# Performance work log

Hardware: AMD Instinct MI355X
Metric: run time of the kernel (lower is better)

## Reference

```python
import jax, jax.numpy as jnp
import numpy as np

B, L, D_IN = 2048, 512, 32
PRED_LEN = 96
COND = 128      # cond_dim (z_dim)
XPROJ = 128     # x_proj_dim defaults to cond_dim
ODE_H = 128     # ode_hidden
TDIM = 128      # time_dim
HID = 256       # hidden of final MLP
N_STEPS = 32    # fixed-step RK4 steps over t in [0,1] (stands in for adaptive dopri5)
LN_EPS = 1e-5


def _linear(x, w, b):
    return x @ w.T + b


def _layernorm(x, g, b):
    mu = jnp.mean(x, axis=-1, keepdims=True)
    var = jnp.var(x, axis=-1, keepdims=True)
    return (x - mu) * jax.lax.rsqrt(var + LN_EPS) * g + b


def _interp(x_seq, t):
    # linear interp over sequence dim: x_seq (B,L,D), scalar t in [0,1] -> (B,D)
    Ls = x_seq.shape[1]
    pos = jnp.clip(t, 0.0, 1.0) * (Ls - 1)
    i0 = jnp.clip(jnp.floor(pos).astype(jnp.int32), 0, Ls - 1)
    i1 = jnp.clip(i0 + 1, 0, Ls - 1)
    w = (pos - i0.astype(pos.dtype))
    x0 = jax.lax.dynamic_index_in_dim(x_seq, i0, axis=1, keepdims=False)
    x1 = jax.lax.dynamic_index_in_dim(x_seq, i1, axis=1, keepdims=False)
    return (1.0 - w) * x0 + w * x1


def setup_inputs() -> dict:
    key = jax.random.key(0)
    ks = jax.random.split(key, 16)

    def kaiming(k, shape):
        return jax.random.normal(k, shape, jnp.float32) * np.float32(np.sqrt(2.0 / shape[-1]))

    IN_F = PRED_LEN * D_IN + COND + TDIM   # 3328
    OUT_F = PRED_LEN * D_IN                # 3072
    return {
        "x_t": jax.random.normal(ks[0], (B, PRED_LEN, D_IN), jnp.float32),
        "past": jax.random.normal(ks[1], (B, L, D_IN), jnp.float32),
        "t": jax.random.randint(ks[2], (B,), 0, 1000),
        "xproj_w": kaiming(ks[3], (XPROJ, D_IN)), "xproj_b": jnp.zeros((XPROJ,), jnp.float32),
        "z0_w": kaiming(ks[4], (COND, XPROJ)), "z0_b": jnp.zeros((COND,), jnp.float32),
        "ln_g": jnp.ones((COND,), jnp.float32), "ln_b": jnp.zeros((COND,), jnp.float32),
        "w1": kaiming(ks[5], (ODE_H, COND + XPROJ)), "b1": jnp.zeros((ODE_H,), jnp.float32),
        "w2": kaiming(ks[6], (ODE_H, ODE_H)), "b2": jnp.zeros((ODE_H,), jnp.float32),
        "w3": kaiming(ks[7], (COND, ODE_H)), "b3": jnp.zeros((COND,), jnp.float32),
        "fw1": kaiming(ks[8], (HID, IN_F)), "fb1": jnp.zeros((HID,), jnp.float32),
        "fw2": kaiming(ks[9], (HID, HID)), "fb2": jnp.zeros((HID,), jnp.float32),
        "fw3": kaiming(ks[10], (OUT_F, HID)), "fb3": jnp.zeros((OUT_F,), jnp.float32),
    }


def _time_emb(t):
    half = TDIM // 2
    freqs = jnp.exp(-np.float32(np.log(10000.0)) * jnp.arange(half, dtype=jnp.float32) / (half - 1))
    args = t.astype(jnp.float32)[:, None] * freqs[None, :]
    return jnp.concatenate([jnp.sin(args), jnp.cos(args)], axis=1)  # (B, TDIM)


def _forward(x_t, past, t, xproj_w, xproj_b, z0_w, z0_b, ln_g, ln_b,
             w1, b1, w2, b2, w3, b3, fw1, fb1, fw2, fb2, fw3, fb3):
    Bn = x_t.shape[0]
    x_seq = _linear(past, xproj_w, xproj_b)           # (B,L,XPROJ)
    z0 = _linear(x_seq[:, 0, :], z0_w, z0_b)          # (B,COND)

    def odef(tt, z):
        xt = _interp(x_seq, tt)                       # (B,XPROJ)
        zn = _layernorm(z, ln_g, ln_b)
        h = jnp.concatenate([zn, xt], axis=-1)
        h = jax.nn.silu(_linear(h, w1, b1))
        h = jax.nn.silu(_linear(h, w2, b2))
        return _linear(h, w3, b3)                     # (B,COND)

    dt = jnp.float32(1.0 / N_STEPS)

    def step(z, tt):
        k1 = odef(tt, z)
        k2 = odef(tt + dt * 0.5, z + dt * 0.5 * k1)
        k3 = odef(tt + dt * 0.5, z + dt * 0.5 * k2)
        k4 = odef(tt + dt, z + dt * k3)
        return z + (dt / 6.0) * (k1 + 2.0 * k2 + 2.0 * k3 + k4), None

    ts = jnp.arange(N_STEPS, dtype=jnp.float32) * dt
    cond, _ = jax.lax.scan(step, z0, ts)              # zT (B,COND)

    temb = _time_emb(t)                               # (B,TDIM)
    x_flat = x_t.reshape(Bn, -1)                      # (B,PRED_LEN*D_IN)
    h = jnp.concatenate([x_flat, cond, temb], axis=1)
    h = jax.nn.silu(_linear(h, fw1, fb1))
    h = jax.nn.silu(_linear(h, fw2, fb2))
    eps = _linear(h, fw3, fb3)
    return eps.reshape(Bn, PRED_LEN, D_IN)


def reference(x_t, past, t, xproj_w, xproj_b, z0_w, z0_b, ln_g, ln_b,
              w1, b1, w2, b2, w3, b3, fw1, fb1, fw2, fb2, fw3, fb3):
    return _forward(x_t, past, t, xproj_w, xproj_b, z0_w, z0_b, ln_g, ln_b,
                    w1, b1, w2, b2, w3, b3, fw1, fb1, fw2, fb2, fw3, fb3)
```

## Files before the change

### kernel.cpp

```cpp
#include <hip/hip_runtime.h>
#include <math.h>

typedef _Float16 h8f16 __attribute__((ext_vector_type(8)));
typedef _Float16 h2f16 __attribute__((ext_vector_type(2)));
typedef float f32x4 __attribute__((ext_vector_type(4)));

#define MFMA16(a, b, c) __builtin_amdgcn_mfma_f32_16x16x32_f16((a), (b), (c), 0, 0, 0)

__device__ __forceinline__ float silu_f(float v) {
    return v * __builtin_amdgcn_rcpf(1.0f + __expf(-v));
}

__device__ __forceinline__ void bar_lds() {
    asm volatile("s_waitcnt lgkmcnt(0)" ::: "memory");
    __builtin_amdgcn_s_barrier();
    __builtin_amdgcn_sched_barrier(0);
}

__global__ __launch_bounds__(512, 1) void fat_kernel(
    const float* __restrict__ past,
    const float* __restrict__ xproj_w, const float* __restrict__ xproj_b,
    const float* __restrict__ z0_w, const float* __restrict__ z0_b,
    const float* __restrict__ ln_g, const float* __restrict__ ln_b,
    const float* __restrict__ w1, const float* __restrict__ b1,
    const float* __restrict__ w2, const float* __restrict__ b2,
    const float* __restrict__ w3, const float* __restrict__ b3,
    const float* __restrict__ x_t, const int* __restrict__ tvals,
    const float* __restrict__ fw1, const float* __restrict__ fw2,
    const float* __restrict__ fw3,
    float* __restrict__ zbuf, _Float16* __restrict__ hcat,
    _Float16* __restrict__ fw1h, _Float16* __restrict__ fw2h,
    _Float16* __restrict__ fw3h)
{
    __shared__ _Float16 hbuf[16][136];
    __shared__ _Float16 h1S[16][136];
    __shared__ _Float16 h2S[16][136];
    __shared__ float    pS[16][33];
    __shared__ float    x0S[16][128];
    __shared__ float    zS0[16][129];

    const int tid = threadIdx.x;

    if (blockIdx.x >= 128) {
        const int fid = blockIdx.x - 128;
        for (long c = fid * 512 + tid; c < 1032192; c += 104 * 512) {
            if (c < 786432) {
                const long b = c / 384, q = (c % 384) * 8;
                const float* s = x_t + b * 3072 + q;
                const f32x4 u0 = *(const f32x4*)s;
                const f32x4 u1 = *(const f32x4*)(s + 4);
                h8f16 v;
#pragma unroll
                for (int j = 0; j < 4; ++j) { v[j] = (_Float16)u0[j]; v[4 + j] = (_Float16)u1[j]; }
                *(h8f16*)&hcat[b * 3328 + q] = v;
            } else if (c < 819200) {
                const long u = c - 786432;
                const long b = u >> 4;
                const int j0 = (int)(u & 15) * 8;
                const float tv = (float)tvals[b];
                h8f16 v;
#pragma unroll
                for (int j = 0; j < 8; ++j) {
                    const int jj  = j0 + j;
                    const int idx = (jj < 64) ? jj : jj - 64;
                    const float fr = expf(-9.210340371976184f * (float)idx * (1.0f / 63.0f));
                    const float a  = tv * fr;
                    v[j] = (_Float16)((jj < 64) ? sinf(a) : cosf(a));
                }
                *(h8f16*)&hcat[b * 3328 + 3200 + j0] = v;
            } else {
                const float* src; _Float16* dst; long off;
                if (c < 925696)      { src = fw1; dst = fw1h; off = (c - 819200) * 8; }
                else if (c < 933888) { src = fw2; dst = fw2h; off = (c - 925696) * 8; }
                else                 { src = fw3; dst = fw3h; off = (c - 933888) * 8; }
                const f32x4 u0 = *(const f32x4*)(src + off);
                const f32x4 u1 = *(const f32x4*)(src + off + 4);
                h8f16 v;
#pragma unroll
                for (int j = 0; j < 4; ++j) { v[j] = (_Float16)u0[j]; v[4 + j] = (_Float16)u1[j]; }
                *(h8f16*)&dst[off] = v;
            }
        }
        return;
    }

    const int wid  = tid >> 6;
    const int lane = tid & 63;
    const int lrow = lane & 15;
    const int lhi  = lane >> 4;
    const int b0   = blockIdx.x * 16;
    const int nc   = wid * 16 + lrow;
    const int koff = lhi * 8;

    h8f16 w1f[4], wcf, w2f[4], w3f[4];
    float b1t, b2r, b3r;
    {
#pragma unroll
        for (int ks = 0; ks < 4; ++ks) {
            h8f16 v1, v2, v3;
#pragma unroll
            for (int j = 0; j < 8; ++j) {
                const int k = ks * 32 + koff + j;
                v1[j] = (_Float16)(w1[nc * 256 + k] * ln_g[k]);
                v2[j] = (_Float16)w2[nc * 128 + k];
                v3[j] = (_Float16)w3[nc * 128 + k];
            }
            w1f[ks] = v1; w2f[ks] = v2; w3f[ks] = v3;
        }
        float wc[8] = {0, 0, 0, 0, 0, 0, 0, 0};
        float bc = 0.0f, bb = 0.0f;
        const float* w1a = w1 + nc * 256;
        const float* w1b = w1a + 128;
#pragma unroll 4
        for (int k = 0; k < 128; ++k) {
            const float a = w1b[k];
            bc += a * xproj_b[k];
            bb += w1a[k] * ln_b[k];
            const float* xr = xproj_w + k * 32 + koff;
#pragma unroll
            for (int j = 0; j < 8; ++j) wc[j] += a * xr[j];
        }
        h8f16 v;
#pragma unroll
        for (int j = 0; j < 8; ++j) v[j] = (_Float16)wc[j];
        wcf = v;
        b1t = b1[nc] + bc + bb;
        b2r = b2[nc]; b3r = b3[nc];
    }

    pS[tid >> 5][tid & 31] = past[(long)(b0 + (tid >> 5)) * 16384 + (tid & 31)];
    __syncthreads();
    {
        const int r  = tid >> 5;
        const int c0 = (tid & 31) * 4;
#pragma unroll
        for (int cc = 0; cc < 4; ++cc) {
            const int kc = c0 + cc;
            float s = xproj_b[kc];
            const float* xr = xproj_w + kc * 32;
#pragma unroll
            for (int c = 0; c < 32; ++c) s += pS[r][c] * xr[c];
            x0S[r][kc] = s;
        }
    }
    __syncthreads();
    {
        const int nn = tid & 127;
        const int r0 = (tid >> 7) * 4;
        for (int p = 0; p < 4; ++p) {
            const int r = r0 + p;
            float s = z0_b[nn];
            const float* zr = z0_w + nn * 128;
            for (int k = 0; k < 128; ++k) s += x0S[r][k] * zr[k];
            zS0[r][nn] = s;
        }
    }
    __syncthreads();

    float zc[4], krk[4];
#pragma unroll
    for (int j = 0; j < 4; ++j) {
        zc[j] = zS0[4 * lhi + j][nc];
        hbuf[4 * lhi + j][nc] = (_Float16)zc[j];
    }

    const float DT = 1.0f / 32.0f;

    f32x4 s0a, s0b, s1a, s1b;
    auto stage = [&](int e) {
        const float pos = (float)e * 7.984375f;
        const int i0 = (int)pos;
        const int i1 = (i0 < 511) ? i0 + 1 : 511;
        const float* base = past + (long)(b0 + lrow) * 16384;
        const float* p0 = base + i0 * 32 + koff;
        const float* p1 = base + i1 * 32 + koff;
        s0a = *(const f32x4*)p0; s0b = *(const f32x4*)(p0 + 4);
        s1a = *(const f32x4*)p1; s1b = *(const f32x4*)(p1 + 4);
    };
    auto blend = [&](int e) -> h8f16 {
        const float pos = (float)e * 7.984375f;
        const float w = pos - floorf(pos);
        h8f16 r;
#pragma unroll
        for (int j = 0; j < 4; ++j) {
            r[j]     = (_Float16)(s0a[j] + w * (s1a[j] - s0a[j]));
            r[4 + j] = (_Float16)(s0b[j] + w * (s1b[j] - s0b[j]));
        }
        return r;
    };

    const h2f16 one2 = {(_Float16)1.0f, (_Float16)1.0f};

    auto phaseA = [&](h8f16 bxc) {
        h8f16 xf[4];
#pragma unroll
        for (int ks = 0; ks < 4; ++ks)
            xf[ks] = *(const h8f16*)&hbuf[lrow][ks * 32 + koff];
        float s0 = 0.f, s1 = 0.f, q0 = 0.f, q1 = 0.f;
#pragma unroll
        for (int ks = 0; ks < 4; ++ks) {
#pragma unroll
            for (int p = 0; p < 4; ++p) {
                const h2f16 x2 = {xf[ks][2 * p], xf[ks][2 * p + 1]};
                if (p & 1) {
                    s1 = __builtin_amdgcn_fdot2(x2, one2, s1, false);
                    q1 = __builtin_amdgcn_fdot2(x2, x2, q1, false);
                } else {
                    s0 = __builtin_amdgcn_fdot2(x2, one2, s0, false);
                    q0 = __builtin_amdgcn_fdot2(x2, x2, q0, false);
                }
            }
        }
        float s = s0 + s1, q = q0 + q1;
        s += __shfl_xor(s, 16); q += __shfl_xor(q, 16);
        s += __shfl_xor(s, 32); q += __shfl_xor(q, 32);
        const float mu  = s * (1.0f / 128.0f);
        const float var = q * (1.0f / 128.0f) - mu * mu;
        const float inv = 1.0f / sqrtf(var + 1e-5f);
        const _Float16 ih = (_Float16)inv;
        const _Float16 mh = (_Float16)(-mu * inv);
        h8f16 ip, mp;
#pragma unroll
        for (int j = 0; j < 8; ++j) { ip[j] = ih; mp[j] = mh; }
        f32x4 acc = {0, 0, 0, 0};
#pragma unroll
        for (int ks = 0; ks < 4; ++ks) {
            const h8f16 az = xf[ks] * ip + mp;
            acc = MFMA16(az, w1f[ks], acc);
        }
        acc = MFMA16(bxc, wcf, acc);
#pragma unroll
        for (int j = 0; j < 4; ++j)
            h1S[4 * lhi + j][nc] = (_Float16)silu_f(acc[j] + b1t);
    };
    auto phaseB = [&]() {
        f32x4 acc = {0, 0, 0, 0};
#pragma unroll
        for (int ks = 0; ks < 4; ++ks) {
            const h8f16 a = *(const h8f16*)&h1S[lrow][ks * 32 + koff];
            acc = MFMA16(a, w2f[ks], acc);
        }
#pragma unroll
        for (int j = 0; j < 4; ++j)
            h2S[4 * lhi + j][nc] = (_Float16)silu_f(acc[j] + b2r);
    };
    auto phaseC = [&]() -> f32x4 {
        f32x4 acc = {0, 0, 0, 0};
#pragma unroll
        for (int ks = 0; ks < 4; ++ks) {
            const h8f16 a = *(const h8f16*)&h2S[lrow][ks * 32 + koff];
            acc = MFMA16(a, w3f[ks], acc);
        }
#pragma unroll
        for (int j = 0; j < 4; ++j) acc[j] += b3r;
        return acc;
    };

    stage(0);
    h8f16 bxc = blend(0);
    __syncthreads();

#pragma unroll 1
    for (int st = 0; st < 32; ++st) {
        const int e1 = 2 * st + 1, e2 = 2 * st + 2;
        phaseA(bxc);
        stage(e1);
        bar_lds();
        phaseB(); bar_lds();
        {
            const f32x4 k = phaseC();
#pragma unroll
            for (int j = 0; j < 4; ++j) {
                krk[j] = k[j];
                hbuf[4 * lhi + j][nc] = (_Float16)(zc[j] + 0.5f * DT * k[j]);
            }
        }
        bar_lds();
        bxc = blend(e1);
        phaseA(bxc); bar_lds();
        phaseB(); bar_lds();
        {
            const f32x4 k = phaseC();
#pragma unroll
            for (int j = 0; j < 4; ++j) {
                krk[j] += 2.0f * k[j];
                hbuf[4 * lhi + j][nc] = (_Float16)(zc[j] + 0.5f * DT * k[j]);
            }
        }
        bar_lds();
        phaseA(bxc);
        stage(e2);
        bar_lds();
        phaseB(); bar_lds();
        {
            const f32x4 k = phaseC();
#pragma unroll
            for (int j = 0; j < 4; ++j) {
                krk[j] += 2.0f * k[j];
                hbuf[4 * lhi + j][nc] = (_Float16)(zc[j] + DT * k[j]);
            }
        }
        bar_lds();
        bxc = blend(e2);
        phaseA(bxc); bar_lds();
        phaseB(); bar_lds();
        {
            const f32x4 k = phaseC();
#pragma unroll
            for (int j = 0; j < 4; ++j) {
                zc[j] += (DT / 6.0f) * (krk[j] + k[j]);
                hbuf[4 * lhi + j][nc] = (_Float16)zc[j];
            }
        }
        bar_lds();
    }

#pragma unroll
    for (int j = 0; j < 4; ++j)
        zbuf[(long)(b0 + 4 * lhi + j) * 128 + nc] = zc[j];
}

__global__ __launch_bounds__(256) void gemm1z_kernel(
    const _Float16* __restrict__ hcat, const float* __restrict__ cond,
    const _Float16* __restrict__ fw1h, const float* __restrict__ fb1,
    _Float16* __restrict__ h1)
{
    __shared__ _Float16 aS[64][40];
    __shared__ _Float16 wS[64][40];
    const int mb = blockIdx.x * 64, nb = blockIdx.y * 64;
    const int tid = threadIdx.x, lane = tid & 63, wq = tid >> 6;
    const int lrow = lane & 15, lhi = lane >> 4;
    f32x4 acc[4];
#pragma unroll
    for (int nt = 0; nt < 4; ++nt) acc[nt] = (f32x4){0, 0, 0, 0};

    const int sr = tid >> 2;
    const int sk = (tid & 3) * 8;

    for (int k0 = 0; k0 < 3328; k0 += 32) {
        if (k0 >= 3072 && k0 < 3200) {
            const float* s = cond + (long)(mb + sr) * 128 + (k0 - 3072) + sk;
            const f32x4 u0 = *(const f32x4*)s;
            const f32x4 u1 = *(const f32x4*)(s + 4);
            h8f16 v;
#pragma unroll
            for (int j = 0; j < 4; ++j) { v[j] = (_Float16)u0[j]; v[4 + j] = (_Float16)u1[j]; }
            *(h8f16*)&aS[sr][sk] = v;
        } else {
            *(h8f16*)&aS[sr][sk] =
                *(const h8f16*)&hcat[(long)(mb + sr) * 3328 + k0 + sk];
        }
        *(h8f16*)&wS[sr][sk] = *(const h8f16*)&fw1h[(long)(nb + sr) * 3328 + k0 + sk];
        __syncthreads();
        const h8f16 a = *(const h8f16*)&aS[wq * 16 + lrow][lhi * 8];
#pragma unroll
        for (int nt = 0; nt < 4; ++nt) {
            const h8f16 bfr = *(const h8f16*)&wS[nt * 16 + lrow][lhi * 8];
            acc[nt] = MFMA16(a, bfr, acc[nt]);
        }
        __syncthreads();
    }

#pragma unroll
    for (int nt = 0; nt < 4; ++nt) {
        const int cc = nb + nt * 16 + lrow;
        const float bv = fb1[cc];
#pragma unroll
        for (int j = 0; j < 4; ++j) {
            const int rr = mb + wq * 16 + lhi * 4 + j;
            h1[(long)rr * 256 + cc] = (_Float16)silu_f(acc[nt][j] + bv);
        }
    }
}

template <bool SILU, bool OUT_F16>
__global__ __launch_bounds__(256) void gemm_ff(
    const _Float16* __restrict__ A, const _Float16* __restrict__ W,
    const float* __restrict__ bias, void* __restrict__ out,
    int M, int N, int K)
{
    __shared__ _Float16 aS[64][40];
    __shared__ _Float16 wS[64][40];
    const int mb = blockIdx.x * 64, nb = blockIdx.y * 64;
    const int tid = threadIdx.x, lane = tid & 63, wq = tid >> 6;
    const int lrow = lane & 15, lhi = lane >> 4;
    f32x4 acc[4];
#pragma unroll
    for (int nt = 0; nt < 4; ++nt) acc[nt] = (f32x4){0, 0, 0, 0};

    const int sr = tid >> 2;
    const int sk = (tid & 3) * 8;

    for (int k0 = 0; k0 < K; k0 += 32) {
        *(h8f16*)&aS[sr][sk] = *(const h8f16*)&A[(long)(mb + sr) * K + k0 + sk];
        *(h8f16*)&wS[sr][sk] = *(const h8f16*)&W[(long)(nb + sr) * K + k0 + sk];
        __syncthreads();
        const h8f16 a = *(const h8f16*)&aS[wq * 16 + lrow][lhi * 8];
#pragma unroll
        for (int nt = 0; nt < 4; ++nt) {
            const h8f16 bfr = *(const h8f16*)&wS[nt * 16 + lrow][lhi * 8];
            acc[nt] = MFMA16(a, bfr, acc[nt]);
        }
        __syncthreads();
    }

#pragma unroll
    for (int nt = 0; nt < 4; ++nt) {
        const int cc = nb + nt * 16 + lrow;
        const float bv = bias[cc];
#pragma unroll
        for (int j = 0; j < 4; ++j) {
            const int rr = mb + wq * 16 + lhi * 4 + j;
            float v = acc[nt][j] + bv;
            if (SILU) v = silu_f(v);
            if (OUT_F16) ((_Float16*)out)[(long)rr * N + cc] = (_Float16)v;
            else         ((float*)out)[(long)rr * N + cc] = v;
        }
    }
}

extern "C" void kernel_launch(void* const* d_in, const int* in_sizes, int n_in,
                              void* d_out, int out_size, void* d_ws, size_t ws_size,
                              hipStream_t stream)
{
    const float* x_t     = (const float*)d_in[0];
    const float* past    = (const float*)d_in[1];
    const int*   tvals   = (const int*)d_in[2];
    const float* xproj_w = (const float*)d_in[3];
    const float* xproj_b = (const float*)d_in[4];
    const float* z0_w    = (const float*)d_in[5];
    const float* z0_b    = (const float*)d_in[6];
    const float* ln_g    = (const float*)d_in[7];
    const float* ln_b    = (const float*)d_in[8];
    const float* w1      = (const float*)d_in[9];
    const float* b1      = (const float*)d_in[10];
    const float* w2      = (const float*)d_in[11];
    const float* b2      = (const float*)d_in[12];
    const float* w3      = (const float*)d_in[13];
    const float* b3      = (const float*)d_in[14];
    const float* fw1     = (const float*)d_in[15];
    const float* fb1     = (const float*)d_in[16];
    const float* fw2     = (const float*)d_in[17];
    const float* fb2     = (const float*)d_in[18];
    const float* fw3     = (const float*)d_in[19];
    const float* fb3     = (const float*)d_in[20];

    char* ws = (char*)d_ws;
    float*     zbuf = (float*)ws;
    _Float16*  hcat = (_Float16*)(ws + (1 << 20));
    _Float16*  h1   = (_Float16*)(ws + 15 * (1 << 20));
    _Float16*  h2   = (_Float16*)(ws + 16 * (1 << 20));
    _Float16*  fw1h = (_Float16*)(ws + 17 * (1 << 20));
    _Float16*  fw2h = (_Float16*)(ws + 19 * (1 << 20));
    _Float16*  fw3h = (_Float16*)(ws + 20 * (1 << 20));

    fat_kernel<<<232, 512, 0, stream>>>(past, xproj_w, xproj_b, z0_w, z0_b,
                                        ln_g, ln_b, w1, b1, w2, b2, w3, b3,
                                        x_t, tvals, fw1, fw2, fw3,
                                        zbuf, hcat, fw1h, fw2h, fw3h);

    gemm1z_kernel<<<dim3(32, 4), 256, 0, stream>>>(hcat, zbuf, fw1h, fb1, h1);

    gemm_ff<true,  true ><<<dim3(32, 4),  256, 0, stream>>>(h1, fw2h, fb2, h2, 2048, 256, 256);
    gemm_ff<false, false><<<dim3(32, 48), 256, 0, stream>>>(h2, fw3h, fb3, d_out, 2048, 3072, 256);
}
```

Baseline: 297.8 us.

## Fuse second and third feed-forward GEMMs with h2 kept in LDS

Merges the two final MLP GEMMs into one kernel. Each block computes the SiLU hidden tile for its 64 rows into shared memory, then streams fw3 tiles against it to write six 64-column output tiles. This drops one kernel launch and the global write and read of h2. In exchange, the 256x256 layer is recomputed once per column-group block, and the output GEMM runs on far fewer blocks with longer serial loops, so there is less parallelism for hiding latency.

After: 315.4 us. 5.9% more time.

```diff
diff --git a/kernel.cpp b/kernel.cpp
--- a/kernel.cpp
+++ b/kernel.cpp
@@ -373,48 +373,73 @@
     }
 }
 
-template <bool SILU, bool OUT_F16>
-__global__ __launch_bounds__(256) void gemm_ff(
-    const _Float16* __restrict__ A, const _Float16* __restrict__ W,
-    const float* __restrict__ bias, void* __restrict__ out,
-    int M, int N, int K)
+__global__ __launch_bounds__(256) void gemm23_kernel(
+    const _Float16* __restrict__ h1, const _Float16* __restrict__ fw2h,
+    const float* __restrict__ fb2, const _Float16* __restrict__ fw3h,
+    const float* __restrict__ fb3, float* __restrict__ out)
 {
     __shared__ _Float16 aS[64][40];
     __shared__ _Float16 wS[64][40];
-    const int mb = blockIdx.x * 64, nb = blockIdx.y * 64;
+    __shared__ _Float16 h2T[64][264];
+    const int mb = blockIdx.x * 64;
+    const int n3base = blockIdx.y * 384;
     const int tid = threadIdx.x, lane = tid & 63, wq = tid >> 6;
     const int lrow = lane & 15, lhi = lane >> 4;
-    f32x4 acc[4];
-#pragma unroll
-    for (int nt = 0; nt < 4; ++nt) acc[nt] = (f32x4){0, 0, 0, 0};
-
     const int sr = tid >> 2;
     const int sk = (tid & 3) * 8;
 
-    for (int k0 = 0; k0 < K; k0 += 32) {
-        *(h8f16*)&aS[sr][sk] = *(const h8f16*)&A[(long)(mb + sr) * K + k0 + sk];
-        *(h8f16*)&wS[sr][sk] = *(const h8f16*)&W[(long)(nb + sr) * K + k0 + sk];
+    for (int nb2 = 0; nb2 < 256; nb2 += 64) {
+        f32x4 acc[4];
+#pragma unroll
+        for (int nt = 0; nt < 4; ++nt) acc[nt] = (f32x4){0, 0, 0, 0};
+        for (int k0 = 0; k0 < 256; k0 += 32) {
+            *(h8f16*)&aS[sr][sk] = *(const h8f16*)&h1[(long)(mb + sr) * 256 + k0 + sk];
+            *(h8f16*)&wS[sr][sk] = *(const h8f16*)&fw2h[(long)(nb2 + sr) * 256 + k0 + sk];
+            __syncthreads();
+            const h8f16 a = *(const h8f16*)&aS[wq * 16 + lrow][lhi * 8];
+#pragma unroll
+            for (int nt = 0; nt < 4; ++nt) {
+                const h8f16 bfr = *(const h8f16*)&wS[nt * 16 + lrow][lhi * 8];
+                acc[nt] = MFMA16(a, bfr, acc[nt]);
+            }
+            __syncthreads();
+        }
+#pragma unroll
+        for (int nt = 0; nt < 4; ++nt) {
+            const int cc = nb2 + nt * 16 + lrow;
+            const float bv = fb2[cc];
+#pragma unroll
+            for (int j = 0; j < 4; ++j)
+                h2T[wq * 16 + lhi * 4 + j][cc] = (_Float16)silu_f(acc[nt][j] + bv);
+        }
         __syncthreads();
-        const h8f16 a = *(const h8f16*)&aS[wq * 16 + lrow][lhi * 8];
+    }
+
+    for (int nt3 = 0; nt3 < 384; nt3 += 64) {
+        const int nb3 = n3base + nt3;
+        f32x4 acc[4];
+#pragma unroll
+        for (int nt = 0; nt < 4; ++nt) acc[nt] = (f32x4){0, 0, 0, 0};
+        for (int k0 = 0; k0 < 256; k0 += 32) {
+            *(h8f16*)&wS[sr][sk] = *(const h8f16*)&fw3h[(long)(nb3 + sr) * 256 + k0 + sk];
+            __syncthreads();
+            const h8f16 a = *(const h8f16*)&h2T[wq * 16 + lrow][k0 + lhi * 8];
+#pragma unroll
+            for (int nt = 0; nt < 4; ++nt) {
+                const h8f16 bfr = *(const h8f16*)&wS[nt * 16 + lrow][lhi * 8];
+                acc[nt] = MFMA16(a, bfr, acc[nt]);
+            }
+            __syncthreads();
+        }
 #pragma unroll
         for (int nt = 0; nt < 4; ++nt) {
-            const h8f16 bfr = *(const h8f16*)&wS[nt * 16 + lrow][lhi * 8];
-            acc[nt] = MFMA16(a, bfr, acc[nt]);
-        }
-        __syncthreads();
-    }
-
-#pragma unroll
-    for (int nt = 0; nt < 4; ++nt) {
-        const int cc = nb + nt * 16 + lrow;
-        const float bv = bias[cc];
-#pragma unroll
-        for (int j = 0; j < 4; ++j) {
-            const int rr = mb + wq * 16 + lhi * 4 + j;
-            float v = acc[nt][j] + bv;
-            if (SILU) v = silu_f(v);
-            if (OUT_F16) ((_Float16*)out)[(long)rr * N + cc] = (_Float16)v;
-            else         ((float*)out)[(long)rr * N + cc] = v;
+            const int cc = nb3 + nt * 16 + lrow;
+            const float bv = fb3[cc];
+#pragma unroll
+            for (int j = 0; j < 4; ++j) {
+                const int rr = mb + wq * 16 + lhi * 4 + j;
+                out[(long)rr * 3072 + cc] = acc[nt][j] + bv;
+            }
         }
     }
 }
@@ -449,7 +474,6 @@
     float*     zbuf = (float*)ws;
     _Float16*  hcat = (_Float16*)(ws + (1 << 20));
     _Float16*  h1   = (_Float16*)(ws + 15 * (1 << 20));
-    _Float16*  h2   = (_Float16*)(ws + 16 * (1 << 20));
     _Float16*  fw1h = (_Float16*)(ws + 17 * (1 << 20));
     _Float16*  fw2h = (_Float16*)(ws + 19 * (1 << 20));
     _Float16*  fw3h = (_Float16*)(ws + 20 * (1 << 20));
@@ -461,6 +485,6 @@
 
     gemm1z_kernel<<<dim3(32, 4), 256, 0, stream>>>(hcat, zbuf, fw1h, fb1, h1);
 
-    gemm_ff<true,  true ><<<dim3(32, 4),  256, 0, stream>>>(h1, fw2h, fb2, h2, 2048, 256, 256);
-    gemm_ff<false, false><<<dim3(32, 48), 256, 0, stream>>>(h2, fw3h, fb3, d_out, 2048, 3072, 256);
-}
+    gemm23_kernel<<<dim3(32, 8), 256, 0, stream>>>(h1, fw2h, fb2, fw3h, fb3,
+                                                   (float*)d_out);
+}
```
